# Kernel optimization log

Measured on AMD Instinct MI355X. Metric: run time of the kernel, lower is better.

The kernel has to match this reference:

```python
import jax, jax.numpy as jnp
import numpy as np

NEG_INF = -1e30  # stands in for float('-inf') masked_fill; safe under softmax
MAX_ITERS = 6


def setup_inputs() -> dict:
    key = jax.random.key(0)
    ks = jax.random.split(key, 8)
    B, T, D, Dp, E = 8, 1500, 1536, 1024, 192
    s = lambda fan_in: 1.0 / np.sqrt(fan_in)
    return {
        "h": jax.random.normal(ks[0], (B, T, D), jnp.float32),
        "W1": jax.random.normal(ks[1], (3 * D, Dp), jnp.float32) * s(3 * D),
        "Wc": jax.random.normal(ks[2], (D, Dp), jnp.float32) * s(D),
        "W2": jax.random.normal(ks[3], (Dp, D), jnp.float32) * s(Dp),
        "b2": jnp.zeros((D,), jnp.float32),
        "w0": jax.random.normal(ks[4], (2 * D, E), jnp.float32) * s(2 * D),
        "b0": jnp.zeros((E,), jnp.float32),
        "Wstop": jax.random.normal(ks[5], (2 * D, 1), jnp.float32) * s(2 * D),
        "bstop": jnp.zeros((1,), jnp.float32),
        "threshold": jnp.full((1,), 0.5, jnp.float32),
        "C0": jnp.zeros((D,), jnp.float32),
    }


def _weighted_stats(h, a):
    # h: [B,T,D], a broadcastable to [B,T,D]
    mu = jnp.sum(a * h, axis=1)                         # [B,D]
    second = jnp.sum(a * h * h, axis=1)                 # [B,D]
    sigma = jnp.sqrt(jnp.clip(second - mu * mu, 1e-8))
    return mu, sigma


def reference(h, W1, Wc, W2, b2, w0, b0, Wstop, bstop, threshold, C0):
    B, T, D = h.shape
    th = threshold[0]

    # a_init = 1/T is constant across iterations -> hoist uniform stats and W1(e)
    mu0, sigma0 = _weighted_stats(h, jnp.float32(1.0 / T))          # [B,D]
    e = jnp.concatenate(
        [h,
         jnp.broadcast_to(mu0[:, None, :], (B, T, D)),
         jnp.broadcast_to(sigma0[:, None, :], (B, T, D))], axis=-1)  # [B,T,3D]
    base = jnp.einsum('btk,kp->btp', e, W1)                          # [B,T,Dp]

    energy_mask = jnp.mean(h * h, axis=-1) > 1e-4                    # [B,T]

    C = jnp.broadcast_to(C0[None, :], (B, D))
    stop = jnp.zeros((B,), bool)
    mask = jnp.ones((B, MAX_ITERS), bool)
    iters = jnp.arange(MAX_ITERS)

    embs, probs = [], []
    for i in range(MAX_ITERS):
        out1 = base + (C @ Wc)[:, None, :]                           # [B,T,Dp]
        out2 = jax.nn.relu(out1) @ W2 + b2                           # [B,T,D]
        att_raw = jnp.mean(out2, axis=-1)                            # [B,T]
        att_raw = jnp.where(energy_mask, att_raw, NEG_INF)
        A = jax.nn.softmax(att_raw, axis=-1)
        A = A / (jnp.sum(A, axis=1, keepdims=True) + 1e-8)

        # NOTE: faithful to source -- second weighted_stats uses out2 ('a'), not A
        mu_p, sigma_p = _weighted_stats(h, out2)                     # [B,D]
        emb = jnp.concatenate([mu_p, sigma_p], axis=-1) @ w0 + b0    # [B,E]
        emb = emb / jnp.maximum(
            jnp.linalg.norm(emb, axis=-1, keepdims=True), 1e-12)

        active = (~stop).astype(h.dtype)[:, None]
        C = C + active * (jnp.einsum('bt,btd->bd', A, h) / T)

        z = jnp.concatenate([jnp.sum(A[:, :, None] * out2, axis=1), C], axis=-1)
        p = jax.nn.sigmoid(z @ Wstop + bstop)[:, 0]                  # [B]

        newly = p < th
        mask = mask & ~(newly[:, None] & (iters[None, :] >= i))
        stop = stop | newly
        embs.append(emb)
        probs.append(p)

    E = jnp.stack(embs, axis=1)                                      # [B,6,E]
    E = E * mask[:, :, None].astype(E.dtype)
    P = jnp.stack(probs, axis=1)                                     # [B,6]
    return E, P
```

## Files before the change

kernel.cpp:

```cpp
#include <hip/hip_runtime.h>
#include <math.h>

#define NB 8
#define NT 1500
#define ND 1536
#define NP 1024
#define NE 192
#define NITER 6
#define NEGINF -1e30f

typedef __attribute__((ext_vector_type(8))) short bf16x8;
typedef __attribute__((ext_vector_type(4))) float f32x4;
typedef __attribute__((ext_vector_type(8))) unsigned short us16x8;

__device__ __forceinline__ unsigned short bf_rne(float x) {
    unsigned u = __float_as_uint(x);
    return (unsigned short)((u + 0x7FFFu + ((u >> 16) & 1u)) >> 16);
}
__device__ __forceinline__ float bf_f(unsigned short u) {
    return __uint_as_float(((unsigned)u) << 16);
}

__device__ __forceinline__ float block_reduce_sum(float v, float* red) {
    int tid = threadIdx.x;
    red[tid] = v; __syncthreads();
    for (int s = blockDim.x >> 1; s > 0; s >>= 1) {
        if (tid < s) red[tid] += red[tid + s];
        __syncthreads();
    }
    float r = red[0]; __syncthreads();
    return r;
}

__global__ void k_colstats(const float* __restrict__ h, float* __restrict__ sum1,
                           float* __restrict__ sum2) {
    int d = blockIdx.x * 256 + threadIdx.x;
    int b = blockIdx.y;
    int t0 = blockIdx.z * 125, t1 = t0 + 125;
    const float* hp = h + (size_t)b * NT * ND + d;
    float s = 0.f, s2 = 0.f;
    for (int t = t0; t < t1; ++t) { float v = hp[(size_t)t * ND]; s += v; s2 += v * v; }
    atomicAdd(&sum1[b * ND + d], s);
    atomicAdd(&sum2[b * ND + d], s2);
}

__global__ void k_stats_fin(float* __restrict__ mu0, float* __restrict__ sig0) {
    int i = blockIdx.x * 256 + threadIdx.x;
    float mu = mu0[i] * (1.f / NT);
    float sec = sig0[i] * (1.f / NT);
    mu0[i] = mu;
    sig0[i] = sqrtf(fmaxf(sec - mu * mu, 1e-8f));
}

__global__ void k_w2r(const float* __restrict__ W2, const float* __restrict__ b2,
                      float* __restrict__ w2r, float* __restrict__ b2m) {
    __shared__ float red[256];
    int p = blockIdx.x;
    float s = 0.f;
    if (p < NP) {
        const float* row = W2 + (size_t)p * ND;
        for (int d = threadIdx.x; d < ND; d += 256) s += row[d];
        s = block_reduce_sum(s, red);
        if (threadIdx.x == 0) w2r[p] = s * (1.f / ND);
    } else {
        for (int d = threadIdx.x; d < ND; d += 256) s += b2[d];
        s = block_reduce_sum(s, red);
        if (threadIdx.x == 0) b2m[0] = s * (1.f / ND);
    }
}

__global__ void k_biasb(const float* __restrict__ W1, const float* __restrict__ mu0,
                        const float* __restrict__ sig0, float* __restrict__ biasb) {
    int p = blockIdx.x * 256 + threadIdx.x;
    int d0 = blockIdx.y * 192, d1 = d0 + 192;
    float acc[NB];
#pragma unroll
    for (int b = 0; b < NB; ++b) acc[b] = 0.f;
    for (int d = d0; d < d1; ++d) {
        float wa = W1[(size_t)(ND + d) * NP + p];
        float wb = W1[(size_t)(2 * ND + d) * NP + p];
#pragma unroll
        for (int b = 0; b < NB; ++b)
            acc[b] += mu0[b * ND + d] * wa + sig0[b * ND + d] * wb;
    }
#pragma unroll
    for (int b = 0; b < NB; ++b) atomicAdd(&biasb[b * NP + p], acc[b]);
}

__global__ void k_init(float* __restrict__ C, const float* __restrict__ C0,
                       float* __restrict__ stopf) {
    int d = blockIdx.x * 256 + threadIdx.x;
    int b = blockIdx.y;
    C[b * ND + d] = C0[d];
    if (blockIdx.x == 0 && threadIdx.x == 0) stopf[b] = 0.f;
}

__global__ void k_split_w(const float* __restrict__ W, int ldw, int kcnt,
                          unsigned short* __restrict__ th, unsigned short* __restrict__ tl) {
    __shared__ float t[128][33];
    int nt = blockIdx.x, kc = blockIdx.y, tid = threadIdx.x;
    int col = tid & 127, kh = tid >> 7;
    const float* wp = W + (size_t)(kc * 32 + kh) * ldw + nt * 128 + col;
#pragma unroll
    for (int i = 0; i < 16; ++i)
        t[col][kh + 2 * i] = wp[(size_t)(2 * i) * ldw];
    __syncthreads();
    int r = tid >> 1;
    int swz = (r >> 1) & 3;
    size_t tb = ((size_t)nt * kcnt + kc) * 4096;
#pragma unroll
    for (int j = 0; j < 2; ++j) {
        int so = (tid & 1) * 2 + j;
        int s = so ^ swz;
        us16x8 hv, lv;
#pragma unroll
        for (int q = 0; q < 8; ++q) {
            float x = t[r][s * 8 + q];
            unsigned short hh = bf_rne(x);
            hv[q] = hh;
            lv[q] = bf_rne(x - bf_f(hh));
        }
        *(us16x8*)&th[tb + r * 32 + so * 8] = hv;
        *(us16x8*)&tl[tb + r * 32 + so * 8] = lv;
    }
}

__global__ void k_split_h(const float* __restrict__ h, unsigned short* __restrict__ th,
                          float* __restrict__ energy) {
    int tr = blockIdx.x, kc = blockIdx.y, b = blockIdx.z;
    int tid = threadIdx.x;
    int r = tid >> 1, quad = tid & 1;
    int row = tr * 128 + r;
    bool ok = row < NT;
    size_t tb = ((size_t)(b * 12 + tr) * 48 + kc) * 4096;
    const float* hp = h + ((size_t)b * NT + (ok ? row : 0)) * ND + kc * 32 + quad * 16;
    int swz = (r >> 1) & 3;
    float es = 0.f;
#pragma unroll
    for (int half = 0; half < 2; ++half) {
        us16x8 hv;
#pragma unroll
        for (int j = 0; j < 2; ++j) {
            float x0 = 0.f, x1 = 0.f, x2 = 0.f, x3 = 0.f;
            if (ok) {
                float4 v = *(const float4*)(hp + half * 8 + j * 4);
                x0 = v.x; x1 = v.y; x2 = v.z; x3 = v.w;
                es += x0 * x0 + x1 * x1 + x2 * x2 + x3 * x3;
            }
            hv[j * 4 + 0] = bf_rne(x0); hv[j * 4 + 1] = bf_rne(x1);
            hv[j * 4 + 2] = bf_rne(x2); hv[j * 4 + 3] = bf_rne(x3);
        }
        int off = r * 32 + (((quad * 2 + half) ^ swz) << 3);
        *(us16x8*)&th[tb + off] = hv;
    }
    es += __shfl_xor(es, 1);
    if (ok && quad == 0) atomicAdd(&energy[b * NT + row], es);
}

__global__ void k_relu_att(const unsigned short* __restrict__ base16,
                           const float* __restrict__ cvec, const float* __restrict__ w2r,
                           unsigned short* __restrict__ th, float* __restrict__ att) {
    int tr = blockIdx.x, kc = blockIdx.y, b = blockIdx.z;
    int tid = threadIdx.x;
    int r = tid >> 1, quad = tid & 1;
    int row = tr * 128 + r;
    bool ok = row < NT;
    size_t tb = ((size_t)(b * 12 + tr) * 32 + kc) * 4096;
    const unsigned short* bp = base16 + ((size_t)b * NT + (ok ? row : 0)) * NP + kc * 32 + quad * 16;
    const float* cv = cvec + b * NP + kc * 32 + quad * 16;
    const float* wr = w2r + kc * 32 + quad * 16;
    int swz = (r >> 1) & 3;
    float asum = 0.f;
#pragma unroll
    for (int half = 0; half < 2; ++half) {
        us16x8 bv = (us16x8){0, 0, 0, 0, 0, 0, 0, 0};
        if (ok) bv = *(const us16x8*)(bp + half * 8);
        us16x8 hv;
#pragma unroll
        for (int j = 0; j < 2; ++j) {
            float4 c4 = *(const float4*)(cv + half * 8 + j * 4);
            float4 w4 = *(const float4*)(wr + half * 8 + j * 4);
            float x0 = fmaxf(bf_f(bv[j * 4 + 0]) + c4.x, 0.f);
            float x1 = fmaxf(bf_f(bv[j * 4 + 1]) + c4.y, 0.f);
            float x2 = fmaxf(bf_f(bv[j * 4 + 2]) + c4.z, 0.f);
            float x3 = fmaxf(bf_f(bv[j * 4 + 3]) + c4.w, 0.f);
            if (ok) asum += x0 * w4.x + x1 * w4.y + x2 * w4.z + x3 * w4.w;
            hv[j * 4 + 0] = bf_rne(x0); hv[j * 4 + 1] = bf_rne(x1);
            hv[j * 4 + 2] = bf_rne(x2); hv[j * 4 + 3] = bf_rne(x3);
        }
        int off = r * 32 + (((quad * 2 + half) ^ swz) << 3);
        *(us16x8*)&th[tb + off] = hv;
    }
    asum += __shfl_xor(asum, 1);
    if (ok && quad == 0) atomicAdd(&att[b * NT + row], asum);
}

__global__ __launch_bounds__(256, 4) void k_gemm_relu(
    const unsigned short* __restrict__ ht, const unsigned short* __restrict__ at_h,
    const unsigned short* __restrict__ bt_h, const float* __restrict__ b2,
    const float* __restrict__ Aw, float* __restrict__ mup, float* __restrict__ s2p,
    float* __restrict__ zab, float* __restrict__ ahb) {
    constexpr int KC2 = NP / 64;
    __shared__ __align__(16) unsigned short As[8192];
    __shared__ __align__(16) unsigned short Bs[8192];
    int flat = blockIdx.x + 12 * (blockIdx.y + 12 * blockIdx.z);
    int swzf = (flat & 7) * 144 + (flat >> 3);
    int tr = swzf % 12, nt = (swzf / 12) % 12, b = swzf / 144;
    int tid = threadIdx.x;
    int lane = tid & 63, w = tid >> 6;
    int wr = w >> 1, wc = w & 1;
    int l15 = lane & 15, kg = lane >> 4;
    int sw = (l15 >> 1) & 3;
    f32x4 acc[4][4];
#pragma unroll
    for (int m = 0; m < 4; ++m)
#pragma unroll
        for (int n = 0; n < 4; ++n) acc[m][n] = (f32x4){0.f, 0.f, 0.f, 0.f};
    int aoff[4], boff[4];
#pragma unroll
    for (int m = 0; m < 4; ++m) aoff[m] = (wr * 64 + m * 16 + l15) * 32 + ((kg ^ sw) << 3);
#pragma unroll
    for (int n = 0; n < 4; ++n) boff[n] = (wc * 64 + n * 16 + l15) * 32 + ((kg ^ sw) << 3);

    const unsigned short* ga = at_h + ((size_t)(b * 12 + tr) * 32) * 4096 + lane * 8;
    const unsigned short* gb = bt_h + ((size_t)nt * 32) * 4096 + lane * 8;

    for (int kc2 = 0; kc2 < KC2; ++kc2) {
#pragma unroll
        for (int c = 0; c < 8; ++c) {
            int seg = w * 8 + c;
            int part = seg & 15, mat = seg >> 4;
            const unsigned short* src = (mat ? gb : ga) + (size_t)kc2 * 8192 + part * 512;
            unsigned short* dst = (mat ? &Bs[0] : &As[0]) + part * 512;
            __builtin_amdgcn_global_load_lds(src, dst, 16, 0, 0);
        }
        __syncthreads();
#pragma unroll
        for (int half = 0; half < 2; ++half) {
            int ho = half * 4096;
            bf16x8 af[4], bfr[4];
#pragma unroll
            for (int m = 0; m < 4; ++m) af[m] = *(const bf16x8*)&As[ho + aoff[m]];
#pragma unroll
            for (int n = 0; n < 4; ++n) bfr[n] = *(const bf16x8*)&Bs[ho + boff[n]];
#pragma unroll
            for (int n = 0; n < 4; ++n)
#pragma unroll
                for (int m = 0; m < 4; ++m)
                    acc[m][n] = __builtin_amdgcn_mfma_f32_16x16x32_bf16(af[m], bfr[n], acc[m][n], 0, 0, 0);
        }
        __syncthreads();
    }

    int rowb = tr * 128 + wr * 64 + (kg << 2);
    int colb = nt * 128 + wc * 64 + l15;
    const unsigned short* htb = ht + (size_t)(b * 12 + tr) * 48 * 4096;
    float b2c[4];
#pragma unroll
    for (int n = 0; n < 4; ++n) b2c[n] = b2[colb + n * 16];
    float pm[4] = {0, 0, 0, 0}, ps2[4] = {0, 0, 0, 0}, pza[4] = {0, 0, 0, 0}, pah[4] = {0, 0, 0, 0};
#pragma unroll
    for (int m = 0; m < 4; ++m) {
#pragma unroll
        for (int q = 0; q < 4; ++q) {
            int row = rowb + m * 16 + q;
            int r_in = wr * 64 + (kg << 2) + m * 16 + q;
            bool ok = row < NT;
            float okf = ok ? 1.f : 0.f;
            float a = Aw[b * NT + (ok ? row : (NT - 1))] * okf;
            int rsw = (r_in >> 1) & 3;
#pragma unroll
            for (int n = 0; n < 4; ++n) {
                int col = colb + n * 16;
                float hv = bf_f(htb[(size_t)(col >> 5) * 4096 + r_in * 32 +
                                    ((((col & 31) >> 3) ^ rsw) << 3) + (col & 7)]) * okf;
                float o2 = acc[m][n][q] + b2c[n];
                pm[n] = fmaf(o2, hv, pm[n]);
                ps2[n] = fmaf(o2 * hv, hv, ps2[n]);
                pza[n] = fmaf(a, o2, pza[n]);
                pah[n] = fmaf(a, hv, pah[n]);
            }
        }
    }
#pragma unroll
    for (int n = 0; n < 4; ++n) {
        pm[n] += __shfl_xor(pm[n], 16); pm[n] += __shfl_xor(pm[n], 32);
        ps2[n] += __shfl_xor(ps2[n], 16); ps2[n] += __shfl_xor(ps2[n], 32);
        pza[n] += __shfl_xor(pza[n], 16); pza[n] += __shfl_xor(pza[n], 32);
        pah[n] += __shfl_xor(pah[n], 16); pah[n] += __shfl_xor(pah[n], 32);
        if (kg == 0) {
            int col = colb + n * 16;
            atomicAdd(&mup[b * ND + col], pm[n]);
            atomicAdd(&s2p[b * ND + col], ps2[n]);
            atomicAdd(&zab[b * ND + col], pza[n]);
            atomicAdd(&ahb[b * ND + col], pah[n]);
        }
    }
}

__global__ __launch_bounds__(256, 3) void k_gemm_base(
    const unsigned short* __restrict__ ht, const unsigned short* __restrict__ bt_h,
    const unsigned short* __restrict__ bt_l, const float* __restrict__ biasb,
    unsigned short* __restrict__ Out16) {
    constexpr int KC2 = ND / 64;
    __shared__ __align__(16) unsigned short As[8192];
    __shared__ __align__(16) unsigned short Bh_s[8192];
    __shared__ __align__(16) unsigned short Bl_s[8192];
    int flat = blockIdx.x + 12 * (blockIdx.y + 8 * blockIdx.z);
    int swzf = (flat & 7) * 96 + (flat >> 3);
    int tr = swzf % 12, nt = (swzf / 12) % 8, b = swzf / 96;
    int tid = threadIdx.x;
    int lane = tid & 63, w = tid >> 6;
    int wr = w >> 1, wc = w & 1;
    int l15 = lane & 15, kg = lane >> 4;
    int sw = (l15 >> 1) & 3;
    f32x4 acc[4][4];
#pragma unroll
    for (int m = 0; m < 4; ++m)
#pragma unroll
        for (int n = 0; n < 4; ++n) acc[m][n] = (f32x4){0.f, 0.f, 0.f, 0.f};
    int aoff[4], boff[4];
#pragma unroll
    for (int m = 0; m < 4; ++m) aoff[m] = (wr * 64 + m * 16 + l15) * 32 + ((kg ^ sw) << 3);
#pragma unroll
    for (int n = 0; n < 4; ++n) boff[n] = (wc * 64 + n * 16 + l15) * 32 + ((kg ^ sw) << 3);

    const unsigned short* ga = ht + ((size_t)(b * 12 + tr) * 48) * 4096 + lane * 8;
    const unsigned short* gbh = bt_h + ((size_t)nt * 48) * 4096 + lane * 8;
    const unsigned short* gbl = bt_l + ((size_t)nt * 48) * 4096 + lane * 8;

    for (int kc2 = 0; kc2 < KC2; ++kc2) {
#pragma unroll
        for (int c = 0; c < 12; ++c) {
            int seg = w * 12 + c;
            int part = seg & 15, mat = seg >> 4;
            const unsigned short* src =
                (mat == 0 ? ga : mat == 1 ? gbh : gbl) + (size_t)kc2 * 8192 + part * 512;
            unsigned short* dst =
                (mat == 0 ? &As[0] : mat == 1 ? &Bh_s[0] : &Bl_s[0]) + part * 512;
            __builtin_amdgcn_global_load_lds(src, dst, 16, 0, 0);
        }
        __syncthreads();
#pragma unroll
        for (int half = 0; half < 2; ++half) {
            int ho = half * 4096;
            bf16x8 af[4];
#pragma unroll
            for (int m = 0; m < 4; ++m) af[m] = *(const bf16x8*)&As[ho + aoff[m]];
#pragma unroll
            for (int n = 0; n < 4; ++n) {
                bf16x8 bh = *(const bf16x8*)&Bh_s[ho + boff[n]];
                bf16x8 bl = *(const bf16x8*)&Bl_s[ho + boff[n]];
#pragma unroll
                for (int m = 0; m < 4; ++m) {
                    acc[m][n] = __builtin_amdgcn_mfma_f32_16x16x32_bf16(af[m], bh, acc[m][n], 0, 0, 0);
                    acc[m][n] = __builtin_amdgcn_mfma_f32_16x16x32_bf16(af[m], bl, acc[m][n], 0, 0, 0);
                }
            }
        }
        __syncthreads();
    }

    int rowb = tr * 128 + wr * 64 + (kg << 2);
    int colb = nt * 128 + wc * 64 + l15;
#pragma unroll
    for (int m = 0; m < 4; ++m)
#pragma unroll
        for (int q = 0; q < 4; ++q) {
            int row = rowb + m * 16 + q;
            if (row < NT) {
                unsigned short* orow = Out16 + ((size_t)b * NT + row) * NP;
#pragma unroll
                for (int n = 0; n < 4; ++n)
                    orow[colb + n * 16] =
                        bf_rne(acc[m][n][q] + biasb[b * NP + colb + n * 16]);
            }
        }
}

__global__ void k_cvec(const float* __restrict__ C, const float* __restrict__ Wc,
                       float* __restrict__ cvec) {
    int p = blockIdx.x * 256 + threadIdx.x;
    int d0 = blockIdx.y * 48, d1 = d0 + 48;
    float acc[NB];
#pragma unroll
    for (int b = 0; b < NB; ++b) acc[b] = 0.f;
    for (int d = d0; d < d1; ++d) {
        float wc = Wc[(size_t)d * NP + p];
#pragma unroll
        for (int b = 0; b < NB; ++b) acc[b] += C[b * ND + d] * wc;
    }
#pragma unroll
    for (int b = 0; b < NB; ++b) atomicAdd(&cvec[b * NP + p], acc[b]);
}

__global__ void k_softmax(const float* __restrict__ att, const float* __restrict__ energy,
                          const float* __restrict__ b2m, float* __restrict__ A) {
    __shared__ float red[256];
    int b = blockIdx.x, tid = threadIdx.x;
    float bm = b2m[0];
    const float* x = att + (size_t)b * NT;
    const float* en = energy + (size_t)b * NT;
    float* a = A + (size_t)b * NT;
    float mx = -3.4e38f;
    for (int t = tid; t < NT; t += 256) {
        float v = (en[t] * (1.f / ND) > 1e-4f) ? x[t] + bm : NEGINF;
        mx = fmaxf(mx, v);
    }
    red[tid] = mx; __syncthreads();
    for (int s = 128; s > 0; s >>= 1) {
        if (tid < s) red[tid] = fmaxf(red[tid], red[tid + s]);
        __syncthreads();
    }
    mx = red[0]; __syncthreads();
    float sm = 0.f;
    for (int t = tid; t < NT; t += 256) {
        float v = (en[t] * (1.f / ND) > 1e-4f) ? x[t] + bm : NEGINF;
        float e = expf(v - mx); a[t] = e; sm += e;
    }
    float s1 = block_reduce_sum(sm, red);
    float inv1 = 1.f / s1;
    float sm2 = 0.f;
    for (int t = tid; t < NT; t += 256) { float v = a[t] * inv1; a[t] = v; sm2 += v; }
    float s2 = block_reduce_sum(sm2, red);
    float inv2 = 1.f / (s2 + 1e-8f);
    for (int t = tid; t < NT; t += 256) a[t] *= inv2;
}

__global__ void k_embacc(const float* __restrict__ red4, const float* __restrict__ w0,
                         float* __restrict__ embt) {
    __shared__ float mus[NB][48], sgs[NB][48];
    int e = threadIdx.x;
    int d0 = blockIdx.x * 48;
    const float* mup = red4;
    const float* s2p = red4 + (size_t)NB * ND;
    for (int idx = e; idx < NB * 48; idx += 192) {
        int b = idx / 48, dd = idx % 48;
        float mu = mup[b * ND + d0 + dd];
        mus[b][dd] = mu;
        sgs[b][dd] = sqrtf(fmaxf(s2p[b * ND + d0 + dd] - mu * mu, 1e-8f));
    }
    __syncthreads();
    float acc[NB];
#pragma unroll
    for (int b = 0; b < NB; ++b) acc[b] = 0.f;
    for (int dd = 0; dd < 48; ++dd) {
        float wa = w0[(size_t)(d0 + dd) * NE + e];
        float wb = w0[(size_t)(ND + d0 + dd) * NE + e];
#pragma unroll
        for (int b = 0; b < NB; ++b)
            acc[b] += mus[b][dd] * wa + sgs[b][dd] * wb;
    }
#pragma unroll
    for (int b = 0; b < NB; ++b) atomicAdd(&embt[b * NE + e], acc[b]);
}

__global__ void k_tail2(const float* __restrict__ red4, const float* __restrict__ embt,
                        const float* __restrict__ b0, const float* __restrict__ Wstop,
                        const float* __restrict__ bstop, const float* __restrict__ thr,
                        float* __restrict__ Cb, float* __restrict__ stopf,
                        float* __restrict__ Eout, float* __restrict__ Pout, int iter) {
    __shared__ float red[256];
    __shared__ float liveflag;
    int b = blockIdx.x, tid = threadIdx.x;
    const float* Ahb = red4 + (size_t)2 * NB * ND + b * ND;
    const float* zAb = red4 + (size_t)3 * NB * ND + b * ND;
    float active = (stopf[b] > 0.5f) ? 0.f : 1.f;
    float dsum = 0.f;
    for (int d = tid; d < ND; d += 256) {
        float Cn = Cb[b * ND + d] + active * (Ahb[d] * (1.f / NT));
        Cb[b * ND + d] = Cn;
        dsum += zAb[d] * Wstop[d] + Cn * Wstop[ND + d];
    }
    float s = block_reduce_sum(dsum, red);
    if (tid == 0) {
        float logit = s + bstop[0];
        float p = 1.f / (1.f + expf(-logit));
        Pout[b * NITER + iter] = p;
        bool newly = p < thr[0];
        if (newly) stopf[b] = 1.f;
        liveflag = (active > 0.5f && !newly) ? 1.f : 0.f;
    }
    __syncthreads();
    float live = liveflag;
    float emb = (tid < NE) ? (embt[b * NE + tid] + b0[tid]) : 0.f;
    float nrm = block_reduce_sum(emb * emb, red);
    float sc = live / fmaxf(sqrtf(nrm), 1e-12f);
    if (tid < NE) Eout[((size_t)b * NITER + iter) * NE + tid] = emb * sc;
}

extern "C" void kernel_launch(void* const* d_in, const int* in_sizes, int n_in,
                              void* d_out, int out_size, void* d_ws, size_t ws_size,
                              hipStream_t stream) {
    const float* h = (const float*)d_in[0];
    const float* W1 = (const float*)d_in[1];
    const float* Wc = (const float*)d_in[2];
    const float* W2 = (const float*)d_in[3];
    const float* b2 = (const float*)d_in[4];
    const float* w0 = (const float*)d_in[5];
    const float* b0 = (const float*)d_in[6];
    const float* Wstop = (const float*)d_in[7];
    const float* bstop = (const float*)d_in[8];
    const float* thr = (const float*)d_in[9];
    const float* C0 = (const float*)d_in[10];

    float* Eout = (float*)d_out;
    float* Pout = Eout + (size_t)NB * NITER * NE;

    char* wsb = (char*)d_ws;
    size_t off = 0;
    auto alloc = [&](size_t bytes) -> void* {
        void* p = wsb + off; off += (bytes + 15) & ~(size_t)15; return p;
    };

    unsigned short* base16 = (unsigned short*)alloc((size_t)NB * NT * NP * 2);
    unsigned short* rel_h = (unsigned short*)alloc((size_t)NB * 12 * 32 * 4096 * 2);
    unsigned short* ht_h = (unsigned short*)alloc((size_t)NB * 12 * 48 * 4096 * 2);
    unsigned short* w1t_h = (unsigned short*)alloc((size_t)8 * 48 * 4096 * 2);
    unsigned short* w1t_l = (unsigned short*)alloc((size_t)8 * 48 * 4096 * 2);
    unsigned short* w2t_h = (unsigned short*)alloc((size_t)12 * 32 * 4096 * 2);
    unsigned short* w2t_l = (unsigned short*)alloc((size_t)12 * 32 * 4096 * 2);
    size_t pz = (size_t)2 * NB * ND + NB * NT + NB * NP;
    float* mu0 = (float*)alloc(pz * 4);
    float* sig0 = mu0 + NB * ND;
    float* energy = sig0 + NB * ND;
    float* biasb = energy + NB * NT;
    float* w2r = (float*)alloc(NP * 4);
    float* b2m = (float*)alloc(16);
    size_t zelems = (size_t)NB * NP + NB * NT + 4 * NB * ND + NB * NE;
    float* cvec = (float*)alloc(zelems * 4);
    float* att = cvec + NB * NP;
    float* red4 = att + NB * NT;
    float* mup = red4;
    float* s2p = red4 + NB * ND;
    float* Ahb = red4 + 2 * NB * ND;
    float* zAb = red4 + 3 * NB * ND;
    float* embt = red4 + 4 * NB * ND;
    float* Abuf = (float*)alloc(NB * NT * 4);
    float* Cb = (float*)alloc(NB * ND * 4);
    float* stopf = (float*)alloc(32);
    size_t zero_bytes = zelems * 4;

    hipMemsetAsync(mu0, 0, pz * 4, stream);
    k_colstats<<<dim3(ND / 256, NB, 12), 256, 0, stream>>>(h, mu0, sig0);
    k_stats_fin<<<dim3(NB * ND / 256), 256, 0, stream>>>(mu0, sig0);
    k_w2r<<<dim3(NP + 1), 256, 0, stream>>>(W2, b2, w2r, b2m);
    k_biasb<<<dim3(NP / 256, 8), 256, 0, stream>>>(W1, mu0, sig0, biasb);
    k_split_w<<<dim3(8, 48), 256, 0, stream>>>(W1, NP, 48, w1t_h, w1t_l);
    k_split_w<<<dim3(12, 32), 256, 0, stream>>>(W2, ND, 32, w2t_h, w2t_l);
    k_split_h<<<dim3(12, 48, NB), 256, 0, stream>>>(h, ht_h, energy);
    k_gemm_base<<<dim3(12, 8, NB), 256, 0, stream>>>(ht_h, w1t_h, w1t_l, biasb, base16);
    k_init<<<dim3(ND / 256, NB), 256, 0, stream>>>(Cb, C0, stopf);

    for (int i = 0; i < NITER; ++i) {
        hipMemsetAsync(cvec, 0, zero_bytes, stream);
        k_cvec<<<dim3(4, 32), 256, 0, stream>>>(Cb, Wc, cvec);
        k_relu_att<<<dim3(12, 32, NB), 256, 0, stream>>>(base16, cvec, w2r, rel_h, att);
        k_softmax<<<dim3(NB), 256, 0, stream>>>(att, energy, b2m, Abuf);
        k_gemm_relu<<<dim3(12, 12, NB), 256, 0, stream>>>(
            ht_h, rel_h, w2t_h, b2, Abuf, mup, s2p, zAb, Ahb);
        k_embacc<<<dim3(32), 192, 0, stream>>>(red4, w0, embt);
        k_tail2<<<dim3(NB), 256, 0, stream>>>(red4, embt, b0, Wstop, bstop, thr,
                                              Cb, stopf, Eout, Pout, i);
    }
}
```

Before: 1.120 ms.

## Double-buffer LDS staging in k_gemm_relu and widen k_biasb grid

The relu GEMM's K loop now uses two 32-wide LDS buffers. The next chunk is loaded asynchronously while MFMAs run on the current one, with one barrier per step instead of two, which is meant to hide global-load latency. Separately, k_biasb splits the D reduction into 96 chunks instead of 8, giving more blocks for parallelism at the cost of more atomics. The pipelined loop relies on the end-of-iteration barrier to order writes into the buffer being reused, and it issues a smaller load batch per sync.

```diff
diff --git a/kernel.cpp b/kernel.cpp
--- a/kernel.cpp
+++ b/kernel.cpp
@@ -72,7 +72,7 @@
 __global__ void k_biasb(const float* __restrict__ W1, const float* __restrict__ mu0,
                         const float* __restrict__ sig0, float* __restrict__ biasb) {
     int p = blockIdx.x * 256 + threadIdx.x;
-    int d0 = blockIdx.y * 192, d1 = d0 + 192;
+    int d0 = blockIdx.y * 16, d1 = d0 + 16;
     float acc[NB];
 #pragma unroll
     for (int b = 0; b < NB; ++b) acc[b] = 0.f;
@@ -200,9 +200,9 @@
     const unsigned short* __restrict__ bt_h, const float* __restrict__ b2,
     const float* __restrict__ Aw, float* __restrict__ mup, float* __restrict__ s2p,
     float* __restrict__ zab, float* __restrict__ ahb) {
-    constexpr int KC2 = NP / 64;
-    __shared__ __align__(16) unsigned short As[8192];
-    __shared__ __align__(16) unsigned short Bs[8192];
+    constexpr int KC = NP / 32;
+    __shared__ __align__(16) unsigned short As[2][4096];
+    __shared__ __align__(16) unsigned short Bs[2][4096];
     int flat = blockIdx.x + 12 * (blockIdx.y + 12 * blockIdx.z);
     int swzf = (flat & 7) * 144 + (flat >> 3);
     int tr = swzf % 12, nt = (swzf / 12) % 12, b = swzf / 144;
@@ -222,34 +222,37 @@
 #pragma unroll
     for (int n = 0; n < 4; ++n) boff[n] = (wc * 64 + n * 16 + l15) * 32 + ((kg ^ sw) << 3);
 
-    const unsigned short* ga = at_h + ((size_t)(b * 12 + tr) * 32) * 4096 + lane * 8;
-    const unsigned short* gb = bt_h + ((size_t)nt * 32) * 4096 + lane * 8;
-
-    for (int kc2 = 0; kc2 < KC2; ++kc2) {
-#pragma unroll
-        for (int c = 0; c < 8; ++c) {
-            int seg = w * 8 + c;
-            int part = seg & 15, mat = seg >> 4;
-            const unsigned short* src = (mat ? gb : ga) + (size_t)kc2 * 8192 + part * 512;
-            unsigned short* dst = (mat ? &Bs[0] : &As[0]) + part * 512;
+    const unsigned short* ga = at_h + ((size_t)(b * 12 + tr) * KC) * 4096 + lane * 8;
+    const unsigned short* gb = bt_h + ((size_t)nt * KC) * 4096 + lane * 8;
+
+    auto stage = [&](int buf, int kc) {
+#pragma unroll
+        for (int c = 0; c < 4; ++c) {
+            int seg = w * 4 + c;
+            int part = seg & 7;
+            const unsigned short* src = ((seg >> 3) == 0 ? ga : gb) + (size_t)kc * 4096 + part * 512;
+            unsigned short* dst = ((seg >> 3) == 0 ? &As[buf][0] : &Bs[buf][0]) + part * 512;
             __builtin_amdgcn_global_load_lds(src, dst, 16, 0, 0);
         }
+    };
+
+    stage(0, 0);
+    __syncthreads();
+    int cur = 0;
+    for (int kc = 0; kc < KC; ++kc) {
+        if (kc + 1 < KC) stage(cur ^ 1, kc + 1);
+        bf16x8 af[4], bfr[4];
+#pragma unroll
+        for (int m = 0; m < 4; ++m) af[m] = *(const bf16x8*)&As[cur][aoff[m]];
+#pragma unroll
+        for (int n = 0; n < 4; ++n) bfr[n] = *(const bf16x8*)&Bs[cur][boff[n]];
+#pragma unroll
+        for (int n = 0; n < 4; ++n)
+#pragma unroll
+            for (int m = 0; m < 4; ++m)
+                acc[m][n] = __builtin_amdgcn_mfma_f32_16x16x32_bf16(af[m], bfr[n], acc[m][n], 0, 0, 0);
         __syncthreads();
-#pragma unroll
-        for (int half = 0; half < 2; ++half) {
-            int ho = half * 4096;
-            bf16x8 af[4], bfr[4];
-#pragma unroll
-            for (int m = 0; m < 4; ++m) af[m] = *(const bf16x8*)&As[ho + aoff[m]];
-#pragma unroll
-            for (int n = 0; n < 4; ++n) bfr[n] = *(const bf16x8*)&Bs[ho + boff[n]];
-#pragma unroll
-            for (int n = 0; n < 4; ++n)
-#pragma unroll
-                for (int m = 0; m < 4; ++m)
-                    acc[m][n] = __builtin_amdgcn_mfma_f32_16x16x32_bf16(af[m], bfr[n], acc[m][n], 0, 0, 0);
-        }
-        __syncthreads();
+        cur ^= 1;
     }
 
     int rowb = tr * 128 + wr * 64 + (kg << 2);
@@ -545,7 +548,7 @@
     k_colstats<<<dim3(ND / 256, NB, 12), 256, 0, stream>>>(h, mu0, sig0);
     k_stats_fin<<<dim3(NB * ND / 256), 256, 0, stream>>>(mu0, sig0);
     k_w2r<<<dim3(NP + 1), 256, 0, stream>>>(W2, b2, w2r, b2m);
-    k_biasb<<<dim3(NP / 256, 8), 256, 0, stream>>>(W1, mu0, sig0, biasb);
+    k_biasb<<<dim3(4, 96), 256, 0, stream>>>(W1, mu0, sig0, biasb);
     k_split_w<<<dim3(8, 48), 256, 0, stream>>>(W1, NP, 48, w1t_h, w1t_l);
     k_split_w<<<dim3(12, 32), 256, 0, stream>>>(W2, ND, 32, w2t_h, w2t_l);
     k_split_h<<<dim3(12, 48, NB), 256, 0, stream>>>(h, ht_h, energy);
```

Measured after the change: 1.066 ms. -4.8%, faster.
